# Kernel tuning notes

Hardware: AMD Instinct MI355X
Metric: run time of the kernel (lower is better)

The kernel has to match this reference:

```python
import jax, jax.numpy as jnp
import numpy as np

B, S, L, C = 256, 3, 4096, 2        # batch, num_slices, slice_length, in_channels
NN, CH, GH, HEADS = 4, 64, 64, 4    # num_nodes, cnn_hidden, gat_hidden, gat_heads
BD = CH * NN // 2                   # CNN branch_dim = 128
TD, TH, TL = 256, 4, 2              # transformer dim / heads / layers
NC = 5
DH = TD // TH


def setup_inputs():
    ks = iter(jax.random.split(jax.random.key(0), 128))
    def rn(shape, s=0.05):
        return jax.random.normal(next(ks), shape, jnp.float32) * s
    def bn(c):  # eval-mode BN params: gamma, beta, running_mean, running_var
        return (jax.random.uniform(next(ks), (2, c)) + 0.5, rn((2, c)),
                rn((2, c)), jax.random.uniform(next(ks), (2, c)) + 0.5)
    inp = {}
    inp['x_t'] = jax.random.normal(next(ks), (B, S, L, C), jnp.float32)
    inp['x_f'] = jax.random.uniform(next(ks), (B, S, L, C), jnp.float32)
    # dual-branch CNN params stacked on leading axis: [0]=time branch, [1]=freq branch
    inp['conv1_w'] = rn((2, 32, C, 15)); inp['conv1_b'] = rn((2, 32))
    inp['bn1_g'], inp['bn1_b'], inp['bn1_m'], inp['bn1_v'] = bn(32)
    inp['conv2_w'] = rn((2, 64, 32, 7)); inp['conv2_b'] = rn((2, 64))
    inp['bn2_g'], inp['bn2_b'], inp['bn2_m'], inp['bn2_v'] = bn(64)
    inp['conv3_w'] = rn((2, BD, 64, 3)); inp['conv3_b'] = rn((2, BD))
    inp['bn3_g'], inp['bn3_b'], inp['bn3_m'], inp['bn3_v'] = bn(BD)
    # PyG GATConv params (lin has no bias; att_src/att_dst per head; output bias)
    inp['gat_lin_w'] = rn((HEADS * GH, CH))
    inp['gat_att_src'] = rn((HEADS, GH)); inp['gat_att_dst'] = rn((HEADS, GH))
    inp['gat_bias'] = rn((HEADS * GH,))
    inp['feat_proj_w'] = rn((TD, NN * GH * HEADS)); inp['feat_proj_b'] = rn((TD,))
    # TransformerEncoder (post-norm, relu), params stacked over TL layers
    inp['tr_in_w'] = rn((TL, 3 * TD, TD)); inp['tr_in_b'] = rn((TL, 3 * TD))
    inp['tr_out_w'] = rn((TL, TD, TD)); inp['tr_out_b'] = rn((TL, TD))
    inp['tr_l1_w'] = rn((TL, 4 * TD, TD)); inp['tr_l1_b'] = rn((TL, 4 * TD))
    inp['tr_l2_w'] = rn((TL, TD, 4 * TD)); inp['tr_l2_b'] = rn((TL, TD))
    inp['tr_ln1_g'] = jnp.ones((TL, TD)); inp['tr_ln1_b'] = jnp.zeros((TL, TD))
    inp['tr_ln2_g'] = jnp.ones((TL, TD)); inp['tr_ln2_b'] = jnp.zeros((TL, TD))
    inp['ta_w'] = rn((1, TD)); inp['ta_b'] = rn((1,))
    inp['fc1_w'] = rn((128, TD)); inp['fc1_b'] = rn((128,))
    inp['fc2_w'] = rn((64, 128)); inp['fc2_b'] = rn((64,))
    inp['fc3_w'] = rn((NC, 64)); inp['fc3_b'] = rn((NC,))
    src = [i for i in range(NN) for j in range(NN) if i != j]
    dst = [j for i in range(NN) for j in range(NN) if i != j]
    inp['edge_index'] = jnp.array([src, dst], jnp.int32)
    return inp


def _conv_bn_relu(x, w, b, g, be, m, v, stride, pad):
    y = jax.lax.conv_general_dilated(x, w, (stride,), [(pad, pad)],
                                     dimension_numbers=('NCH', 'OIH', 'NCH'))
    y = (y + b[None, :, None] - m[None, :, None]) * (g / jnp.sqrt(v + 1e-5))[None, :, None] + be[None, :, None]
    return jax.nn.relu(y)


def _branch(x, c1w, c1b, g1, b1, m1, v1, c2w, c2b, g2, b2, m2, v2, c3w, c3b, g3, b3, m3, v3):
    y = _conv_bn_relu(x, c1w, c1b, g1, b1, m1, v1, 2, 7)
    y = _conv_bn_relu(y, c2w, c2b, g2, b2, m2, v2, 2, 3)
    y = _conv_bn_relu(y, c3w, c3b, g3, b3, m3, v3, 1, 1)
    return y.mean(axis=-1)  # AdaptiveAvgPool1d(1)


def _ln(x, g, b):
    mu = x.mean(-1, keepdims=True)
    var = ((x - mu) ** 2).mean(-1, keepdims=True)
    return (x - mu) / jnp.sqrt(var + 1e-5) * g + b


def _model(edge_index, x_t, x_f, conv1_w, conv1_b, bn1_g, bn1_b, bn1_m, bn1_v,
           conv2_w, conv2_b, bn2_g, bn2_b, bn2_m, bn2_v,
           conv3_w, conv3_b, bn3_g, bn3_b, bn3_m, bn3_v,
           gat_lin_w, gat_att_src, gat_att_dst, gat_bias,
           feat_proj_w, feat_proj_b,
           tr_in_w, tr_in_b, tr_out_w, tr_out_b, tr_l1_w, tr_l1_b, tr_l2_w, tr_l2_b,
           tr_ln1_g, tr_ln1_b, tr_ln2_g, tr_ln2_b,
           ta_w, ta_b, fc1_w, fc1_b, fc2_w, fc2_b, fc3_w, fc3_b):
    G = B * S  # fold (batch, slice) -> one big conv/GAT batch (replaces the python loops)
    xt = x_t.transpose(0, 1, 3, 2).reshape(G, C, L)
    xf = x_f.transpose(0, 1, 3, 2).reshape(G, C, L)
    xs = jnp.stack([xt, xf])  # [2, G, C, L]
    pooled = jax.vmap(_branch)(xs, conv1_w, conv1_b, bn1_g, bn1_b, bn1_m, bn1_v,
                               conv2_w, conv2_b, bn2_g, bn2_b, bn2_m, bn2_v,
                               conv3_w, conv3_b, bn3_g, bn3_b, bn3_m, bn3_v)  # [2, G, BD]
    feat = jnp.concatenate([pooled[0], pooled[1]], axis=1).reshape(G, NN, CH)
    # GATConv (dense over the tiny 4-node graph; softmax over in-edges per dest node)
    h = jnp.einsum('gnc,oc->gno', feat, gat_lin_w).reshape(G, NN, HEADS, GH)
    a_src = jnp.einsum('gnhd,hd->gnh', h, gat_att_src)
    a_dst = jnp.einsum('gnhd,hd->gnh', h, gat_att_dst)
    scores = jax.nn.leaky_relu(a_dst[:, :, None, :] + a_src[:, None, :, :], 0.2)  # [G,i,j,H]
    adj = jnp.zeros((NN, NN), bool).at[edge_index[1], edge_index[0]].set(True)
    adj = adj.at[jnp.arange(NN), jnp.arange(NN)].set(True)  # PyG adds self-loops
    alpha = jax.nn.softmax(jnp.where(adj[None, :, :, None], scores, -1e9), axis=2)
    gat_out = jnp.einsum('gijh,gjhd->gihd', alpha, h).reshape(G, NN, HEADS * GH) + gat_bias
    sl = gat_out.reshape(B, S, NN * HEADS * GH) @ feat_proj_w.T + feat_proj_b  # [B,S,TD]
    # positional encoding
    pos = jnp.arange(S, dtype=jnp.float32)[:, None]
    div = jnp.exp(jnp.arange(0, TD, 2, dtype=jnp.float32) * (-np.log(10000.0) / TD))
    pe = jnp.zeros((S, TD)).at[:, 0::2].set(jnp.sin(pos * div)).at[:, 1::2].set(jnp.cos(pos * div))
    x = sl + pe[None]
    # TransformerEncoder, post-norm, relu FFN
    for l in range(TL):
        qkv = x @ tr_in_w[l].T + tr_in_b[l]
        q, k, v = jnp.split(qkv, 3, axis=-1)
        q = q.reshape(B, S, TH, DH).transpose(0, 2, 1, 3)
        k = k.reshape(B, S, TH, DH).transpose(0, 2, 1, 3)
        v = v.reshape(B, S, TH, DH).transpose(0, 2, 1, 3)
        attn = jax.nn.softmax(jnp.einsum('bhqd,bhkd->bhqk', q, k) / np.sqrt(DH), axis=-1)
        a = jnp.einsum('bhqk,bhkd->bhqd', attn, v).transpose(0, 2, 1, 3).reshape(B, S, TD)
        a = a @ tr_out_w[l].T + tr_out_b[l]
        x = _ln(x + a, tr_ln1_g[l], tr_ln1_b[l])
        f = jax.nn.relu(x @ tr_l1_w[l].T + tr_l1_b[l]) @ tr_l2_w[l].T + tr_l2_b[l]
        x = _ln(x + f, tr_ln2_g[l], tr_ln2_b[l])
    w = jax.nn.softmax((x @ ta_w.T + ta_b)[..., 0], axis=1)  # [B,S] temporal attention
    ctx = jnp.einsum('bs,bsd->bd', w, x)
    o = jax.nn.relu(ctx @ fc1_w.T + fc1_b)
    o = jax.nn.relu(o @ fc2_w.T + fc2_b)
    return o @ fc3_w.T + fc3_b  # logits [B, NC]


def reference(x_t, x_f, conv1_w, conv1_b, bn1_g, bn1_b, bn1_m, bn1_v, conv2_w, conv2_b, bn2_g, bn2_b, bn2_m, bn2_v, conv3_w, conv3_b, bn3_g, bn3_b, bn3_m, bn3_v, gat_lin_w, gat_att_src, gat_att_dst, gat_bias, feat_proj_w, feat_proj_b, tr_in_w, tr_in_b, tr_out_w, tr_out_b, tr_l1_w, tr_l1_b, tr_l2_w, tr_l2_b, tr_ln1_g, tr_ln1_b, tr_ln2_g, tr_ln2_b, ta_w, ta_b, fc1_w, fc1_b, fc2_w, fc2_b, fc3_w, fc3_b, edge_index):
    return _model(edge_index, x_t, x_f, conv1_w, conv1_b, bn1_g, bn1_b, bn1_m, bn1_v,
                  conv2_w, conv2_b, bn2_g, bn2_b, bn2_m, bn2_v,
                  conv3_w, conv3_b, bn3_g, bn3_b, bn3_m, bn3_v,
                  gat_lin_w, gat_att_src, gat_att_dst, gat_bias,
                  feat_proj_w, feat_proj_b,
                  tr_in_w, tr_in_b, tr_out_w, tr_out_b, tr_l1_w, tr_l1_b, tr_l2_w, tr_l2_b,
                  tr_ln1_g, tr_ln1_b, tr_ln2_g, tr_ln2_b,
                  ta_w, ta_b, fc1_w, fc1_b, fc2_w, fc2_b, fc3_w, fc3_b)
```

## Files before the change

kernel.cpp:

```cpp
#include <hip/hip_runtime.h>
#include <math.h>

#define Bn 256
#define Sn 3
#define Ln 4096
#define Gn 768
#define TDn 256
#define TLn 2

#define WS_W1K   0
#define WS_W2K   1024
#define WS_W3K   15360
#define WS_H1    39936
#define WS_H2    40000
#define WS_H3    40128
#define WS_FPWH  40960
#define WS_INWH  172032
#define WS_OUTWH 368640
#define WS_L1WH  434176
#define WS_L2WH  696320
#define WS_POOL  958464
#define WS_XH    958464
#define WS_ABH   1056768
#define WS_SCR   1155072
#define WS_Y     1548288
#define WS_X     1744896

typedef _Float16 f16x8 __attribute__((ext_vector_type(8)));
typedef float f32x4 __attribute__((ext_vector_type(4)));
#define MFMA16(a,b,c) __builtin_amdgcn_mfma_f32_16x16x32_f16(a,b,c,0,0,0)

__global__ __launch_bounds__(256) void prep_kernel(
    const float* __restrict__ w1, const float* __restrict__ w2, const float* __restrict__ w3,
    const float* __restrict__ c1b, const float* __restrict__ g1, const float* __restrict__ b1,
    const float* __restrict__ m1, const float* __restrict__ v1,
    const float* __restrict__ c2b, const float* __restrict__ g2, const float* __restrict__ b2,
    const float* __restrict__ m2, const float* __restrict__ v2,
    const float* __restrict__ c3b, const float* __restrict__ g3, const float* __restrict__ b3,
    const float* __restrict__ m3, const float* __restrict__ v3,
    float* __restrict__ ws)
{
    int i = blockIdx.x * 256 + threadIdx.x;
    _Float16* w1k = (_Float16*)(ws + WS_W1K);
    _Float16* w2k = (_Float16*)(ws + WS_W2K);
    _Float16* w3k = (_Float16*)(ws + WS_W3K);
    if (i < 2048) {
        int k = i & 31, oc = (i >> 5) & 31, br = i >> 10;
        int c = k >> 4, tau = k & 15;
        int a = br * 32 + oc;
        float s = g1[a] / sqrtf(v1[a] + 1e-5f);
        float v = (tau < 15) ? w1[(((size_t)a * 2 + c) * 15) + tau] * s : 0.f;
        w1k[i] = (_Float16)v;
    }
    if (i < 28672) {
        int k = i % 224; int a = i / 224;
        int tblk = k >> 5, ic = k & 31;
        int t = (tblk < 4) ? 2 * tblk : 2 * (tblk - 4) + 1;
        float s = g2[a] / sqrtf(v2[a] + 1e-5f);
        w2k[i] = (_Float16)(w2[((size_t)a * 32 + ic) * 7 + t] * s);
    }
    if (i < 49152) {
        int k = i % 192; int a = i / 192;
        int t = k >> 6, ic = k & 63;
        float s = g3[a] / sqrtf(v3[a] + 1e-5f);
        w3k[i] = (_Float16)(w3[((size_t)a * 64 + ic) * 3 + t] * s);
    }
    if (i < 64)  { float s = g1[i] / sqrtf(v1[i] + 1e-5f); ws[WS_H1 + i] = (c1b[i] - m1[i]) * s + b1[i]; }
    if (i < 128) { float s = g2[i] / sqrtf(v2[i] + 1e-5f); ws[WS_H2 + i] = (c2b[i] - m2[i]) * s + b2[i]; }
    if (i < 256) { float s = g3[i] / sqrtf(v3[i] + 1e-5f); ws[WS_H3 + i] = (c3b[i] - m3[i]) * s + b3[i]; }
}

__global__ __launch_bounds__(256) void prep_tr_kernel(
    const float* __restrict__ fpw, const float* __restrict__ inw,
    const float* __restrict__ outw, const float* __restrict__ l1w,
    const float* __restrict__ l2w, float* __restrict__ ws)
{
    int i = blockIdx.x * 256 + threadIdx.x;
    _Float16* fpwh = (_Float16*)(ws + WS_FPWH);
    _Float16* inwh = (_Float16*)(ws + WS_INWH);
    _Float16* outwh = (_Float16*)(ws + WS_OUTWH);
    _Float16* l1wh = (_Float16*)(ws + WS_L1WH);
    _Float16* l2wh = (_Float16*)(ws + WS_L2WH);
    if (i < 262144) fpwh[i] = (_Float16)fpw[i];
    if (i < 393216) inwh[i] = (_Float16)inw[i];
    if (i < 131072) outwh[i] = (_Float16)outw[i];
    if (i < 524288) { l1wh[i] = (_Float16)l1w[i]; l2wh[i] = (_Float16)l2w[i]; }
}

__global__ __launch_bounds__(256, 4) void conv_mfma_kernel(
    const float* __restrict__ x_t, const float* __restrict__ x_f,
    const float* __restrict__ ws, float* __restrict__ pooled)
{
    __shared__ _Float16 xsf[2 * 576];
    __shared__ _Float16 y1[2][132 * 32];
    __shared__ _Float16 y2s[128 * 64];
    __shared__ float h1s[32];
    __shared__ float h2s[64];
    __shared__ float h3s[128];
    __shared__ float pbuf[128];

    const int g = blockIdx.x, br = blockIdx.y;
    const int tid = threadIdx.x;
    const int lane = tid & 63, wv = tid >> 6;
    const int l15 = lane & 15, q4 = lane >> 4;

    const float* xin = (br == 0 ? x_t : x_f) + (size_t)g * (Ln * 2);
    const _Float16* w1k = (const _Float16*)(ws + WS_W1K) + br * 1024;
    const _Float16* w2k = (const _Float16*)(ws + WS_W2K) + br * 14336;
    const _Float16* w3k = (const _Float16*)(ws + WS_W3K) + br * 24576;

    if (tid < 32)  h1s[tid] = ws[WS_H1 + br * 32 + tid];
    if (tid < 64)  h2s[tid] = ws[WS_H2 + br * 64 + tid];
    if (tid < 128) { h3s[tid] = ws[WS_H3 + br * 128 + tid]; pbuf[tid] = 0.f; }

    f16x8 a1[2];
    #pragma unroll
    for (int mt = 0; mt < 2; ++mt)
        a1[mt] = *(const f16x8*)(w1k + (mt * 16 + l15) * 32 + q4 * 8);

    const int mg = wv & 1, ng = wv >> 1;

    const _Float16* w2row = w2k + (size_t)l15 * 224 + q4 * 8;
    const _Float16* w3row = w3k + (size_t)(mg * 64 + l15) * 192 + q4 * 8;

    float pool_[4][4];
    #pragma unroll
    for (int mt = 0; mt < 4; ++mt)
        #pragma unroll
        for (int r = 0; r < 4; ++r) pool_[mt][r] = 0.f;

    const f32x4 vzero = {0.f, 0.f, 0.f, 0.f};

    #pragma unroll 1
    for (int tile = 0; tile < 9; ++tile) {
        const int P0 = tile * 126;
        const int Q0 = 2 * P0 - 5;
        const int x0 = 4 * P0 - 17;

        for (int l = tid; l < 576; l += 256) {
            int xl = x0 + l;
            float a = 0.f, b = 0.f;
            if (xl >= 0 && xl < Ln) { float2 v = *(const float2*)(xin + (size_t)xl * 2); a = v.x; b = v.y; }
            xsf[l] = (_Float16)a; xsf[576 + l] = (_Float16)b;
        }
        __syncthreads();

        const uint* xsu = (const uint*)xsf;
        #pragma unroll 1
        for (int nt = wv; nt < 17; nt += 4) {
            int j0 = nt * 16 + l15;
            union { f16x8 v; uint u[4]; } bf;
            int ubase = (q4 >> 1) * 288 + j0 + (q4 & 1) * 4;
            #pragma unroll
            for (int ii = 0; ii < 4; ++ii) bf.u[ii] = xsu[ubase + ii];
            f32x4 c1acc[2] = {vzero, vzero};
            c1acc[0] = MFMA16(a1[0], bf.v, c1acc[0]);
            c1acc[1] = MFMA16(a1[1], bf.v, c1acc[1]);

            if (j0 <= 260) {
                int q = Q0 + j0;
                bool val = (q >= 0) && (q < 2048);
                int i = j0 >> 1, par = j0 & 1;
                #pragma unroll
                for (int mt = 0; mt < 2; ++mt) {
                    int oc0 = mt * 16 + q4 * 4;
                    union { _Float16 h[4]; uint2 u; } pk;
                    #pragma unroll
                    for (int r = 0; r < 4; ++r) {
                        float y = c1acc[mt][r] + h1s[oc0 + r];
                        y = y > 0.f ? y : 0.f;
                        pk.h[r] = val ? (_Float16)y : (_Float16)0.f;
                    }
                    int gq = mt * 2 + (q4 >> 1), sub = q4 & 1;
                    *(uint2*)(&y1[par][(i * 4 + (gq ^ (i & 3))) * 8 + sub * 4]) = pk.u;
                }
            }
        }
        __syncthreads();

        #pragma unroll 1
        for (int jj = 0; jj < 2; ++jj) {
            f32x4 c2[4] = {vzero, vzero, vzero, vzero};
            f16x8 a2c[4];
            #pragma unroll
            for (int mt = 0; mt < 4; ++mt)
                a2c[mt] = *(const f16x8*)(w2row + (size_t)mt * 16 * 224);
            const int n = wv * 32 + jj * 16 + l15;
            #pragma unroll 1
            for (int ks = 0; ks < 7; ++ks) {
                int roff = (ks < 4) ? ks : ks - 4;
                const _Float16* yb = y1[(ks < 4) ? 0 : 1];
                int i = n + roff;
                f16x8 bb = *(const f16x8*)(yb + (i * 4 + (q4 ^ (i & 3))) * 8);
                f16x8 a2n[4];
                if (ks < 6) {
                    #pragma unroll
                    for (int mt = 0; mt < 4; ++mt)
                        a2n[mt] = *(const f16x8*)(w2row + (size_t)mt * 16 * 224 + (ks + 1) * 32);
                }
                #pragma unroll
                for (int mt = 0; mt < 4; ++mt)
                    c2[mt] = MFMA16(a2c[mt], bb, c2[mt]);
                if (ks < 6) {
                    #pragma unroll
                    for (int mt = 0; mt < 4; ++mt) a2c[mt] = a2n[mt];
                }
            }
            int p2 = P0 - 1 + n;
            bool val = (p2 >= 0) && (p2 < 1024);
            #pragma unroll
            for (int mt = 0; mt < 4; ++mt) {
                int oc0 = mt * 16 + q4 * 4;
                union { _Float16 h[4]; uint2 u; } pk;
                #pragma unroll
                for (int r = 0; r < 4; ++r) {
                    float y = c2[mt][r] + h2s[oc0 + r];
                    y = y > 0.f ? y : 0.f;
                    pk.h[r] = val ? (_Float16)y : (_Float16)0.f;
                }
                int gq = oc0 >> 3, sub = q4 & 1;
                *(uint2*)(&y2s[(n * 8 + (gq ^ (n & 7))) * 8 + sub * 4]) = pk.u;
            }
        }
        __syncthreads();

        #pragma unroll 1
        for (int half = 0; half < 2; ++half) {
            f32x4 c3[4][2];
            #pragma unroll
            for (int mt = 0; mt < 4; ++mt) { c3[mt][0] = vzero; c3[mt][1] = vzero; }
            f16x8 a3c[4];
            #pragma unroll
            for (int mt = 0; mt < 4; ++mt)
                a3c[mt] = *(const f16x8*)(w3row + (size_t)mt * 16 * 192);
            #pragma unroll 1
            for (int ks = 0; ks < 6; ++ks) {
                int t = ks >> 1, ich = ks & 1;
                f16x8 b3[2];
                #pragma unroll
                for (int jj = 0; jj < 2; ++jj) {
                    int np = ng * 64 + (half * 2 + jj) * 16 + l15;
                    int r = np + t; r = r < 128 ? r : 127;
                    int gq3 = ich * 4 + q4;
                    b3[jj] = *(const f16x8*)(&y2s[(r * 8 + (gq3 ^ (r & 7))) * 8]);
                }
                f16x8 a3n[4];
                if (ks < 5) {
                    #pragma unroll
                    for (int mt = 0; mt < 4; ++mt)
                        a3n[mt] = *(const f16x8*)(w3row + (size_t)mt * 16 * 192 + (ks + 1) * 32);
                }
                #pragma unroll
                for (int mt = 0; mt < 4; ++mt) {
                    c3[mt][0] = MFMA16(a3c[mt], b3[0], c3[mt][0]);
                    c3[mt][1] = MFMA16(a3c[mt], b3[1], c3[mt][1]);
                }
                if (ks < 5) {
                    #pragma unroll
                    for (int mt = 0; mt < 4; ++mt) a3c[mt] = a3n[mt];
                }
            }
            #pragma unroll
            for (int mt = 0; mt < 4; ++mt) {
                int oc0 = mg * 64 + mt * 16 + q4 * 4;
                #pragma unroll
                for (int jj = 0; jj < 2; ++jj) {
                    int np = ng * 64 + (half * 2 + jj) * 16 + l15;
                    int p3 = P0 + np;
                    float valf = ((np < 126) && (p3 < 1024)) ? 1.f : 0.f;
                    #pragma unroll
                    for (int r = 0; r < 4; ++r) {
                        float y = c3[mt][jj][r] + h3s[oc0 + r];
                        y = y > 0.f ? y : 0.f;
                        pool_[mt][r] = fmaf(y, valf, pool_[mt][r]);
                    }
                }
            }
        }
        __syncthreads();
    }

    #pragma unroll
    for (int mt = 0; mt < 4; ++mt)
        #pragma unroll
        for (int r = 0; r < 4; ++r) {
            float v = pool_[mt][r];
            v += __shfl_xor(v, 1, 64);
            v += __shfl_xor(v, 2, 64);
            v += __shfl_xor(v, 4, 64);
            v += __shfl_xor(v, 8, 64);
            if (l15 == 0) atomicAdd(&pbuf[mg * 64 + mt * 16 + q4 * 4 + r], v);
        }
    __syncthreads();
    if (tid < 128) pooled[g * 256 + br * 128 + tid] = pbuf[tid] * (1.f / 1024.f);
}

__global__ __launch_bounds__(256) void gat_kernel(
    const float* __restrict__ glw, const float* __restrict__ att_src,
    const float* __restrict__ att_dst, const float* __restrict__ gbias,
    const float* __restrict__ pooled, _Float16* __restrict__ gouth)
{
    __shared__ float feats[256];
    __shared__ float hs[4 * 256];
    __shared__ float av[32];
    __shared__ float alpha[64];

    int g = blockIdx.x, tid = threadIdx.x;
    feats[tid] = pooled[g * 256 + tid];
    __syncthreads();

    {
        int o = tid;
        const float* w = glw + o * 64;
        float a0 = 0, a1 = 0, a2 = 0, a3 = 0;
        for (int c = 0; c < 64; ++c) {
            float wvv = w[c];
            a0 = fmaf(feats[c],       wvv, a0);
            a1 = fmaf(feats[64 + c],  wvv, a1);
            a2 = fmaf(feats[128 + c], wvv, a2);
            a3 = fmaf(feats[192 + c], wvv, a3);
        }
        hs[o] = a0; hs[256 + o] = a1; hs[512 + o] = a2; hs[768 + o] = a3;
    }
    __syncthreads();

    if (tid < 32) {
        int n = (tid & 15) >> 2, hd = tid & 3;
        const float* aw = (tid < 16) ? att_src : att_dst;
        float s = 0;
        for (int d = 0; d < 64; ++d) s = fmaf(hs[n * 256 + hd * 64 + d], aw[hd * 64 + d], s);
        av[tid] = s;
    }
    __syncthreads();

    if (tid < 16) {
        int i = tid >> 2, hd = tid & 3;
        float sc[4], mx = -1e30f;
        #pragma unroll
        for (int j = 0; j < 4; ++j) {
            float v = av[16 + i * 4 + hd] + av[j * 4 + hd];
            v = v > 0.f ? v : 0.2f * v;
            sc[j] = v; mx = fmaxf(mx, v);
        }
        float den = 0;
        #pragma unroll
        for (int j = 0; j < 4; ++j) { sc[j] = expf(sc[j] - mx); den += sc[j]; }
        #pragma unroll
        for (int j = 0; j < 4; ++j) alpha[(i * 4 + j) * 4 + hd] = sc[j] / den;
    }
    __syncthreads();

    {
        int o = tid, hd = o >> 6;
        #pragma unroll
        for (int i = 0; i < 4; ++i) {
            float acc = gbias[o];
            #pragma unroll
            for (int j = 0; j < 4; ++j) acc = fmaf(alpha[(i * 4 + j) * 4 + hd], hs[j * 256 + o], acc);
            gouth[(size_t)g * 1024 + i * 256 + o] = (_Float16)acc;
        }
    }
}

template <int K, int MODE>
__global__ __launch_bounds__(256) void mfma_gemm_kernel(
    const _Float16* __restrict__ A, const _Float16* __restrict__ W,
    const float* __restrict__ bias, float* __restrict__ out32,
    _Float16* __restrict__ out16, int N)
{
    const int tid = threadIdx.x;
    const int wv = tid >> 6, l15 = tid & 15, q4 = (tid & 63) >> 4;
    const int m0 = blockIdx.x * 64 + wv * 16;
    const int n0 = blockIdx.y * 64;

    const f32x4 vzero = {0.f, 0.f, 0.f, 0.f};
    f32x4 acc[4] = {vzero, vzero, vzero, vzero};

    const _Float16* arow = A + (size_t)(m0 + l15) * K + q4 * 8;
    #pragma unroll 4
    for (int ks = 0; ks < K / 32; ++ks) {
        f16x8 a = *(const f16x8*)(arow + ks * 32);
        #pragma unroll
        for (int nt = 0; nt < 4; ++nt) {
            f16x8 b = *(const f16x8*)(W + (size_t)(n0 + nt * 16 + l15) * K + ks * 32 + q4 * 8);
            acc[nt] = MFMA16(a, b, acc[nt]);
        }
    }

    #pragma unroll
    for (int nt = 0; nt < 4; ++nt) {
        int n = n0 + nt * 16 + l15;
        float bs = bias[n];
        #pragma unroll
        for (int r = 0; r < 4; ++r) {
            int m = m0 + q4 * 4 + r;
            float v = acc[nt][r] + bs;
            if (MODE == 1) v = fmaxf(v, 0.f);
            if (MODE == 3) {
                int s = m % 3;
                int kk = n >> 1;
                float dv = expf((float)kk * -0.07195588f);
                float arg = (float)s * dv;
                v += (n & 1) ? cosf(arg) : sinf(arg);
            }
            if (MODE == 0 || MODE == 3) out32[(size_t)m * N + n] = v;
            if (MODE == 1 || MODE == 3) out16[(size_t)m * N + n] = (_Float16)v;
        }
    }
}

template <int K>
__global__ __launch_bounds__(256) void gemm_ln_kernel(
    const _Float16* __restrict__ A, const _Float16* __restrict__ W,
    const float* __restrict__ bias,
    const float* __restrict__ gamma, const float* __restrict__ beta,
    float* __restrict__ X, _Float16* __restrict__ XH)
{
    __shared__ float ys[16][260];
    const int tid = threadIdx.x;
    const int wv = tid >> 6, l15 = tid & 15, q4 = (tid & 63) >> 4;
    const int r0 = blockIdx.x * 16;
    const int n0 = wv * 64;

    const f32x4 vzero = {0.f, 0.f, 0.f, 0.f};
    f32x4 acc[4] = {vzero, vzero, vzero, vzero};

    const _Float16* arow = A + (size_t)(r0 + l15) * K + q4 * 8;
    #pragma unroll 4
    for (int ks = 0; ks < K / 32; ++ks) {
        f16x8 a = *(const f16x8*)(arow + ks * 32);
        #pragma unroll
        for (int nt = 0; nt < 4; ++nt) {
            f16x8 b = *(const f16x8*)(W + (size_t)(n0 + nt * 16 + l15) * K + ks * 32 + q4 * 8);
            acc[nt] = MFMA16(a, b, acc[nt]);
        }
    }

    #pragma unroll
    for (int nt = 0; nt < 4; ++nt) {
        int col = n0 + nt * 16 + l15;
        float bs = bias[col];
        #pragma unroll
        for (int r = 0; r < 4; ++r) {
            int rowl = q4 * 4 + r;
            ys[rowl][col] = acc[nt][r] + bs + X[(size_t)(r0 + rowl) * 256 + col];
        }
    }
    __syncthreads();

    {
        int row = tid >> 4, l16 = tid & 15;
        float s = 0, s2 = 0;
        #pragma unroll
        for (int c0 = 0; c0 < 256; c0 += 16) {
            float v = ys[row][c0 + l16]; s += v; s2 += v * v;
        }
        s += __shfl_xor(s, 1, 64);  s2 += __shfl_xor(s2, 1, 64);
        s += __shfl_xor(s, 2, 64);  s2 += __shfl_xor(s2, 2, 64);
        s += __shfl_xor(s, 4, 64);  s2 += __shfl_xor(s2, 4, 64);
        s += __shfl_xor(s, 8, 64);  s2 += __shfl_xor(s2, 8, 64);
        float mu = s * (1.f / 256.f);
        float var = s2 * (1.f / 256.f) - mu * mu;
        float inv = 1.0f / sqrtf(var + 1e-5f);
        #pragma unroll
        for (int c0 = 0; c0 < 256; c0 += 16) {
            int c = c0 + l16;
            float v = (ys[row][c] - mu) * inv * gamma[c] + beta[c];
            X[(size_t)(r0 + row) * 256 + c] = v;
            XH[(size_t)(r0 + row) * 256 + c] = (_Float16)v;
        }
    }
}

__global__ __launch_bounds__(256) void attn_kernel(
    const float* __restrict__ qkv, _Float16* __restrict__ abufh)
{
    int b = blockIdx.x, tid = threadIdx.x, head = tid >> 6, d = tid & 63;
    const float* base = qkv + (size_t)b * 3 * 768 + head * 64 + d;
    float q[3], k[3], v[3];
    #pragma unroll
    for (int s = 0; s < 3; ++s) {
        const float* row = base + s * 768;
        q[s] = row[0]; k[s] = row[256]; v[s] = row[512];
    }
    float sc[3][3];
    #pragma unroll
    for (int si = 0; si < 3; ++si)
        #pragma unroll
        for (int sj = 0; sj < 3; ++sj) {
            float p = q[si] * k[sj];
            #pragma unroll
            for (int m = 32; m > 0; m >>= 1) p += __shfl_xor(p, m, 64);
            sc[si][sj] = p * 0.125f;
        }
    #pragma unroll
    for (int si = 0; si < 3; ++si) {
        float mx = fmaxf(sc[si][0], fmaxf(sc[si][1], sc[si][2]));
        float e0 = expf(sc[si][0] - mx), e1 = expf(sc[si][1] - mx), e2 = expf(sc[si][2] - mx);
        float den = e0 + e1 + e2;
        float o = (e0 * v[0] + e1 * v[1] + e2 * v[2]) / den;
        abufh[(size_t)(b * 3 + si) * 256 + head * 64 + d] = (_Float16)o;
    }
}

__global__ __launch_bounds__(256) void head_kernel(
    const float* __restrict__ X, const float* __restrict__ taw, const float* __restrict__ tab,
    const float* __restrict__ f1w, const float* __restrict__ f1b,
    const float* __restrict__ f2w, const float* __restrict__ f2b,
    const float* __restrict__ f3w, const float* __restrict__ f3b,
    float* __restrict__ out)
{
    __shared__ float xs[3 * 256];
    __shared__ float wsm[3];
    __shared__ float cs[256];
    __shared__ float a1[128];
    __shared__ float a2[64];
    int b = blockIdx.x, tid = threadIdx.x;
    for (int idx = tid; idx < 768; idx += 256) xs[idx] = X[(size_t)b * 768 + idx];
    __syncthreads();
    if (tid < 3) {
        float s = tab[0];
        for (int d = 0; d < 256; ++d) s = fmaf(xs[tid * 256 + d], taw[d], s);
        wsm[tid] = s;
    }
    __syncthreads();
    {
        float m = fmaxf(wsm[0], fmaxf(wsm[1], wsm[2]));
        float e0 = expf(wsm[0] - m), e1 = expf(wsm[1] - m), e2 = expf(wsm[2] - m);
        float den = e0 + e1 + e2;
        cs[tid] = (e0 * xs[tid] + e1 * xs[256 + tid] + e2 * xs[512 + tid]) / den;
    }
    __syncthreads();
    if (tid < 128) {
        float a = f1b[tid];
        const float* w = f1w + tid * 256;
        for (int c = 0; c < 256; ++c) a = fmaf(cs[c], w[c], a);
        a1[tid] = fmaxf(a, 0.f);
    }
    __syncthreads();
    if (tid < 64) {
        float a = f2b[tid];
        const float* w = f2w + tid * 128;
        for (int c = 0; c < 128; ++c) a = fmaf(a1[c], w[c], a);
        a2[tid] = fmaxf(a, 0.f);
    }
    __syncthreads();
    if (tid < 5) {
        float a = f3b[tid];
        const float* w = f3w + tid * 64;
        for (int c = 0; c < 64; ++c) a = fmaf(a2[c], w[c], a);
        out[b * 5 + tid] = a;
    }
}

extern "C" void kernel_launch(void* const* d_in, const int* in_sizes, int n_in,
                              void* d_out, int out_size, void* d_ws, size_t ws_size,
                              hipStream_t stream) {
    const float* x_t     = (const float*)d_in[0];
    const float* x_f     = (const float*)d_in[1];
    const float* conv1_w = (const float*)d_in[2];
    const float* conv1_b = (const float*)d_in[3];
    const float* bn1_g   = (const float*)d_in[4];
    const float* bn1_b   = (const float*)d_in[5];
    const float* bn1_m   = (const float*)d_in[6];
    const float* bn1_v   = (const float*)d_in[7];
    const float* conv2_w = (const float*)d_in[8];
    const float* conv2_b = (const float*)d_in[9];
    const float* bn2_g   = (const float*)d_in[10];
    const float* bn2_b   = (const float*)d_in[11];
    const float* bn2_m   = (const float*)d_in[12];
    const float* bn2_v   = (const float*)d_in[13];
    const float* conv3_w = (const float*)d_in[14];
    const float* conv3_b = (const float*)d_in[15];
    const float* bn3_g   = (const float*)d_in[16];
    const float* bn3_b   = (const float*)d_in[17];
    const float* bn3_m   = (const float*)d_in[18];
    const float* bn3_v   = (const float*)d_in[19];
    const float* gat_lin_w   = (const float*)d_in[20];
    const float* gat_att_src = (const float*)d_in[21];
    const float* gat_att_dst = (const float*)d_in[22];
    const float* gat_bias    = (const float*)d_in[23];
    const float* feat_proj_w = (const float*)d_in[24];
    const float* feat_proj_b = (const float*)d_in[25];
    const float* tr_in_w  = (const float*)d_in[26];
    const float* tr_in_b  = (const float*)d_in[27];
    const float* tr_out_w = (const float*)d_in[28];
    const float* tr_out_b = (const float*)d_in[29];
    const float* tr_l1_w  = (const float*)d_in[30];
    const float* tr_l1_b  = (const float*)d_in[31];
    const float* tr_l2_w  = (const float*)d_in[32];
    const float* tr_l2_b  = (const float*)d_in[33];
    const float* tr_ln1_g = (const float*)d_in[34];
    const float* tr_ln1_b = (const float*)d_in[35];
    const float* tr_ln2_g = (const float*)d_in[36];
    const float* tr_ln2_b = (const float*)d_in[37];
    const float* ta_w  = (const float*)d_in[38];
    const float* ta_b  = (const float*)d_in[39];
    const float* fc1_w = (const float*)d_in[40];
    const float* fc1_b = (const float*)d_in[41];
    const float* fc2_w = (const float*)d_in[42];
    const float* fc2_b = (const float*)d_in[43];
    const float* fc3_w = (const float*)d_in[44];
    const float* fc3_b = (const float*)d_in[45];

    float* ws    = (float*)d_ws;
    float* POOL  = ws + WS_POOL;
    float* X     = ws + WS_X;
    float* QKV   = ws + WS_SCR;
    _Float16* GOUTH = (_Float16*)(ws + WS_SCR);
    _Float16* MIDH  = (_Float16*)(ws + WS_SCR);
    _Float16* XH    = (_Float16*)(ws + WS_XH);
    _Float16* ABH   = (_Float16*)(ws + WS_ABH);
    const _Float16* FPWH  = (const _Float16*)(ws + WS_FPWH);
    const _Float16* INWH  = (const _Float16*)(ws + WS_INWH);
    const _Float16* OUTWH = (const _Float16*)(ws + WS_OUTWH);
    const _Float16* L1WH  = (const _Float16*)(ws + WS_L1WH);
    const _Float16* L2WH  = (const _Float16*)(ws + WS_L2WH);
    float* out = (float*)d_out;

    prep_kernel<<<192, 256, 0, stream>>>(conv1_w, conv2_w, conv3_w,
        conv1_b, bn1_g, bn1_b, bn1_m, bn1_v,
        conv2_b, bn2_g, bn2_b, bn2_m, bn2_v,
        conv3_b, bn3_g, bn3_b, bn3_m, bn3_v, ws);
    prep_tr_kernel<<<2048, 256, 0, stream>>>(feat_proj_w, tr_in_w, tr_out_w,
                                             tr_l1_w, tr_l2_w, ws);

    conv_mfma_kernel<<<dim3(Gn, 2), 256, 0, stream>>>(x_t, x_f, ws, POOL);

    gat_kernel<<<Gn, 256, 0, stream>>>(gat_lin_w, gat_att_src, gat_att_dst, gat_bias,
                                       POOL, GOUTH);

    mfma_gemm_kernel<1024, 3><<<dim3(12, 4), 256, 0, stream>>>(
        GOUTH, FPWH, feat_proj_b, X, XH, 256);

    for (int l = 0; l < TLn; ++l) {
        mfma_gemm_kernel<256, 0><<<dim3(12, 12), 256, 0, stream>>>(
            XH, INWH + (size_t)l * 196608, tr_in_b + l * 768, QKV, nullptr, 768);
        attn_kernel<<<Bn, 256, 0, stream>>>(QKV, ABH);
        gemm_ln_kernel<256><<<48, 256, 0, stream>>>(
            ABH, OUTWH + (size_t)l * 65536, tr_out_b + l * 256,
            tr_ln1_g + l * 256, tr_ln1_b + l * 256, X, XH);
        mfma_gemm_kernel<256, 1><<<dim3(12, 16), 256, 0, stream>>>(
            XH, L1WH + (size_t)l * 262144, tr_l1_b + l * 1024, nullptr, MIDH, 1024);
        gemm_ln_kernel<1024><<<48, 256, 0, stream>>>(
            MIDH, L2WH + (size_t)l * 262144, tr_l2_b + l * 256,
            tr_ln2_g + l * 256, tr_ln2_b + l * 256, X, XH);
    }

    head_kernel<<<Bn, 256, 0, stream>>>(X, ta_w, ta_b, fc1_w, fc1_b,
                                        fc2_w, fc2_b, fc3_w, fc3_b, out);
}
```

Before: 883.0 us.

## Reuse conv2 weight fragments across both column tiles and drop prefetch buffers

```diff
diff --git a/kernel.cpp b/kernel.cpp
--- a/kernel.cpp
+++ b/kernel.cpp
@@ -87,7 +87,7 @@
     if (i < 524288) { l1wh[i] = (_Float16)l1w[i]; l2wh[i] = (_Float16)l2w[i]; }
 }
 
-__global__ __launch_bounds__(256, 4) void conv_mfma_kernel(
+__global__ __launch_bounds__(256, 3) void conv_mfma_kernel(
     const float* __restrict__ x_t, const float* __restrict__ x_f,
     const float* __restrict__ ws, float* __restrict__ pooled)
 {
@@ -178,48 +178,49 @@
         }
         __syncthreads();
 
-        #pragma unroll 1
-        for (int jj = 0; jj < 2; ++jj) {
-            f32x4 c2[4] = {vzero, vzero, vzero, vzero};
-            f16x8 a2c[4];
+        {
+            f32x4 c2[4][2];
             #pragma unroll
-            for (int mt = 0; mt < 4; ++mt)
-                a2c[mt] = *(const f16x8*)(w2row + (size_t)mt * 16 * 224);
-            const int n = wv * 32 + jj * 16 + l15;
+            for (int mt = 0; mt < 4; ++mt) { c2[mt][0] = vzero; c2[mt][1] = vzero; }
             #pragma unroll 1
             for (int ks = 0; ks < 7; ++ks) {
                 int roff = (ks < 4) ? ks : ks - 4;
                 const _Float16* yb = y1[(ks < 4) ? 0 : 1];
-                int i = n + roff;
-                f16x8 bb = *(const f16x8*)(yb + (i * 4 + (q4 ^ (i & 3))) * 8);
-                f16x8 a2n[4];
-                if (ks < 6) {
-                    #pragma unroll
-                    for (int mt = 0; mt < 4; ++mt)
-                        a2n[mt] = *(const f16x8*)(w2row + (size_t)mt * 16 * 224 + (ks + 1) * 32);
+                f16x8 a2f[4];
+                #pragma unroll
+                for (int mt = 0; mt < 4; ++mt)
+                    a2f[mt] = *(const f16x8*)(w2row + (size_t)mt * 16 * 224 + ks * 32);
+                f16x8 bb[2];
+                #pragma unroll
+                for (int jj = 0; jj < 2; ++jj) {
+                    int n = wv * 32 + jj * 16 + l15;
+                    int i = n + roff;
+                    bb[jj] = *(const f16x8*)(yb + (i * 4 + (q4 ^ (i & 3))) * 8);
                 }
                 #pragma unroll
-                for (int mt = 0; mt < 4; ++mt)
-                    c2[mt] = MFMA16(a2c[mt], bb, c2[mt]);
-                if (ks < 6) {
-                    #pragma unroll
-                    for (int mt = 0; mt < 4; ++mt) a2c[mt] = a2n[mt];
+                for (int mt = 0; mt < 4; ++mt) {
+                    c2[mt][0] = MFMA16(a2f[mt], bb[0], c2[mt][0]);
+                    c2[mt][1] = MFMA16(a2f[mt], bb[1], c2[mt][1]);
                 }
             }
-            int p2 = P0 - 1 + n;
-            bool val = (p2 >= 0) && (p2 < 1024);
             #pragma unroll
-            for (int mt = 0; mt < 4; ++mt) {
-                int oc0 = mt * 16 + q4 * 4;
-                union { _Float16 h[4]; uint2 u; } pk;
-                #pragma unroll
-                for (int r = 0; r < 4; ++r) {
-                    float y = c2[mt][r] + h2s[oc0 + r];
-                    y = y > 0.f ? y : 0.f;
-                    pk.h[r] = val ? (_Float16)y : (_Float16)0.f;
+            for (int jj = 0; jj < 2; ++jj) {
+                int n = wv * 32 + jj * 16 + l15;
+                int p2 = P0 - 1 + n;
+                bool val = (p2 >= 0) && (p2 < 1024);
+                #pragma unroll
+                for (int mt = 0; mt < 4; ++mt) {
+                    int oc0 = mt * 16 + q4 * 4;
+                    union { _Float16 h[4]; uint2 u; } pk;
+                    #pragma unroll
+                    for (int r = 0; r < 4; ++r) {
+                        float y = c2[mt][jj][r] + h2s[oc0 + r];
+                        y = y > 0.f ? y : 0.f;
+                        pk.h[r] = val ? (_Float16)y : (_Float16)0.f;
+                    }
+                    int gq = oc0 >> 3, sub = q4 & 1;
+                    *(uint2*)(&y2s[(n * 8 + (gq ^ (n & 7))) * 8 + sub * 4]) = pk.u;
                 }
-                int gq = oc0 >> 3, sub = q4 & 1;
-                *(uint2*)(&y2s[(n * 8 + (gq ^ (n & 7))) * 8 + sub * 4]) = pk.u;
             }
         }
         __syncthreads();
@@ -229,13 +230,13 @@
             f32x4 c3[4][2];
             #pragma unroll
             for (int mt = 0; mt < 4; ++mt) { c3[mt][0] = vzero; c3[mt][1] = vzero; }
-            f16x8 a3c[4];
-            #pragma unroll
-            for (int mt = 0; mt < 4; ++mt)
-                a3c[mt] = *(const f16x8*)(w3row + (size_t)mt * 16 * 192);
             #pragma unroll 1
             for (int ks = 0; ks < 6; ++ks) {
                 int t = ks >> 1, ich = ks & 1;
+                f16x8 a3f[4];
+                #pragma unroll
+                for (int mt = 0; mt < 4; ++mt)
+                    a3f[mt] = *(const f16x8*)(w3row + (size_t)mt * 16 * 192 + ks * 32);
                 f16x8 b3[2];
                 #pragma unroll
                 for (int jj = 0; jj < 2; ++jj) {
@@ -244,20 +245,10 @@
                     int gq3 = ich * 4 + q4;
                     b3[jj] = *(const f16x8*)(&y2s[(r * 8 + (gq3 ^ (r & 7))) * 8]);
                 }
-                f16x8 a3n[4];
-                if (ks < 5) {
-                    #pragma unroll
-                    for (int mt = 0; mt < 4; ++mt)
-                        a3n[mt] = *(const f16x8*)(w3row + (size_t)mt * 16 * 192 + (ks + 1) * 32);
-                }
                 #pragma unroll
                 for (int mt = 0; mt < 4; ++mt) {
-                    c3[mt][0] = MFMA16(a3c[mt], b3[0], c3[mt][0]);
-                    c3[mt][1] = MFMA16(a3c[mt], b3[1], c3[mt][1]);
-                }
-                if (ks < 5) {
-                    #pragma unroll
-                    for (int mt = 0; mt < 4; ++mt) a3c[mt] = a3n[mt];
+                    c3[mt][0] = MFMA16(a3f[mt], b3[0], c3[mt][0]);
+                    c3[mt][1] = MFMA16(a3f[mt], b3[1], c3[mt][1]);
                 }
             }
             #pragma unroll
```

Result: faster. 776.9 us (-12.0%).
